# Kernel tuning notes

Measured on AMD Instinct MI355X. Metric: run time of the kernel, lower is better.

## Reference

```python
import jax, jax.numpy as jnp
import numpy as np

B = 64
N_TEXT, N_VIS, N_AC = 256, 32, 32
N = N_TEXT + N_VIS + N_AC  # 320 total graph nodes
HID, HEADS, LAYERS = 512, 8, 2
HEAD_DIM = HID // HEADS
SW_K, SW_P, SF_M, ALPHA, CROSS_P = 6, 0.15, 3, 0.5, 0.3


def build_hybrid_adj():
    """Watts-Strogatz + Barabasi-Albert hybrid adjacency with cross-modal edges (numpy, setup only)."""
    rng = np.random.default_rng(0)
    # small-world ring lattice
    sw = np.zeros((N, N), np.float32)
    idx = np.arange(N)
    for j in range(1, SW_K // 2 + 1):
        sw[idx, (idx + j) % N] = 1.0
        sw[idx, (idx - j) % N] = 1.0
    # rewiring
    for i in range(N):
        for j in range(i + 1, N):
            if sw[i, j] == 1 and rng.random() < SW_P:
                sw[i, j] = sw[j, i] = 0.0
                cand = np.where(sw[i] == 0)[0]
                cand = cand[cand != i]
                if len(cand) > 0:
                    nj = rng.choice(cand)
                    sw[i, nj] = sw[nj, i] = 1.0
    # scale-free (Barabasi-Albert)
    sf = np.zeros((N, N), np.float32)
    for i in range(SF_M + 1):
        for j in range(i + 1, SF_M + 1):
            sf[i, j] = sf[j, i] = 1.0
    deg = sf.sum(1)
    for v in range(SF_M + 1, N):
        prob = deg[:v] / deg[:v].sum()
        targets = rng.choice(v, size=min(SF_M, v), replace=False, p=prob)
        sf[v, targets] = 1.0
        sf[targets, v] = 1.0
        deg = sf.sum(1)
    adj = ((ALPHA * sw + (1.0 - ALPHA) * sf) > 0.3).astype(np.float32)
    # cross-modal edges: text<->visual, text<->acoustic (Bernoulli), visual<->acoustic temporal diagonal
    ts, te = 0, N_TEXT
    vs, ve = te, te + N_VIS
    as_, ae = ve, ve + N_AC
    cm_v = (rng.random((N_TEXT, N_VIS)) < CROSS_P).astype(np.float32)
    adj[ts:te, vs:ve] = np.maximum(adj[ts:te, vs:ve], cm_v)
    adj[vs:ve, ts:te] = adj[ts:te, vs:ve].T
    cm_a = (rng.random((N_TEXT, N_AC)) < CROSS_P).astype(np.float32)
    adj[ts:te, as_:ae] = np.maximum(adj[ts:te, as_:ae], cm_a)
    adj[as_:ae, ts:te] = adj[ts:te, as_:ae].T
    k = min(N_VIS, N_AC)
    adj[vs + np.arange(k), as_ + np.arange(k)] = 1.0
    adj[as_ + np.arange(k), vs + np.arange(k)] = 1.0
    return adj.astype(np.int32)


def setup_inputs() -> dict:
    key = jax.random.key(0)
    ks = jax.random.split(key, 12)
    s = 0.02
    return {
        "text": jax.random.normal(ks[0], (B, N_TEXT, 768), jnp.float32),
        "visual": jax.random.normal(ks[1], (B, N_VIS, 47), jnp.float32),
        "acoustic": jax.random.normal(ks[2], (B, N_AC, 74), jnp.float32),
        "adj": jnp.asarray(build_hybrid_adj()),
        "Wt": jax.random.normal(ks[3], (768, HID), jnp.float32) * s,
        "Wv": jax.random.normal(ks[4], (47, HID), jnp.float32) * s,
        "Wa": jax.random.normal(ks[5], (74, HID), jnp.float32) * s,
        "Wg": jax.random.normal(ks[6], (LAYERS, HEADS, HID, HEAD_DIM), jnp.float32) * s,
        "a_src": jax.random.normal(ks[7], (LAYERS, HEADS, HEAD_DIM), jnp.float32) * s,
        "a_dst": jax.random.normal(ks[8], (LAYERS, HEADS, HEAD_DIM), jnp.float32) * s,
        "edge_logits": jax.random.normal(ks[9], (N, N), jnp.float32) * s,
    }


def _fusion(text, visual, acoustic, adj, Wt, Wv, Wa, Wg, a_src, a_dst, edge_logits):
    # project each modality into shared hidden space and stack as graph nodes
    x = jnp.concatenate([
        jnp.einsum("btd,dh->bth", text, Wt),
        jnp.einsum("bvd,dh->bvh", visual, Wv),
        jnp.einsum("bad,dh->bah", acoustic, Wa),
    ], axis=1)  # [B, N, HID]
    mask = (adj != 0)[None, None, :, :]  # [1,1,N,N]
    for l in range(LAYERS):
        h = jnp.einsum("bnd,hdf->bhnf", x, Wg[l])          # [B,H,N,Fh]
        # a([h_i || h_j]) factorizes: e_ij = a_src.h_i + a_dst.h_j
        fi = jnp.einsum("bhnf,hf->bhn", h, a_src[l])
        fj = jnp.einsum("bhnf,hf->bhn", h, a_dst[l])
        e = jax.nn.leaky_relu(fi[:, :, :, None] + fj[:, :, None, :], 0.2)
        e = e + edge_logits[None, None, :, :]               # learnable topology bias
        e = jnp.where(mask, e, -jnp.inf)                    # adjacency-masked scores
        att = jnp.nan_to_num(jax.nn.softmax(e, axis=-1))    # fully-masked rows -> 0
        out = jnp.einsum("bhij,bhjf->bhif", att, h)         # message passing
        x = out.transpose(0, 2, 1, 3).reshape(x.shape[0], N, HID)  # concat heads
        if l < LAYERS - 1:
            x = jax.nn.elu(x)
    return x  # [B, N, HID] fused node embeddings


def reference(text, visual, acoustic, adj, Wt, Wv, Wa, Wg, a_src, a_dst, edge_logits):
    return _fusion(text, visual, acoustic, adj, Wt, Wv, Wa, Wg, a_src, a_dst, edge_logits)
```

## Files before the change

### kernel.cpp

```cpp
#include <hip/hip_runtime.h>
#include <hip/hip_bf16.h>
#include <math.h>

#define BB 64
#define NN 320
#define NT 256
#define NV 32
#define NA 32
#define HIDD 512
#define NHEAD 8
#define FD 64

typedef __attribute__((ext_vector_type(8))) short bf16x8;
typedef __attribute__((ext_vector_type(4))) float floatx4;

__device__ float me_g[NN * NN];
__device__ float fif_g[512 * NN];
__device__ float fjf_g[512 * NN];
__device__ unsigned short tihi_g[16384 * 768];
__device__ unsigned short tilo_g[16384 * 768];
__device__ unsigned short vihi_g[2048 * 64];
__device__ unsigned short vilo_g[2048 * 64];
__device__ unsigned short achi_g[2048 * 128];
__device__ unsigned short aclo_g[2048 * 128];
__device__ unsigned short xhi_g[20480 * 512];
__device__ unsigned short xlo_g[20480 * 512];
__device__ unsigned short bwhi_g[512 * 768];
__device__ unsigned short bwlo_g[512 * 768];

__device__ __forceinline__ void split1(float v, unsigned short& h, unsigned short& l) {
    unsigned u = __float_as_uint(v);
    unsigned hu = u & 0xFFFF0000u;
    float lf = v - __uint_as_float(hu);
    h = (unsigned short)(hu >> 16);
    l = (unsigned short)(__float_as_uint(lf) >> 16);
}
__device__ __forceinline__ unsigned pack2(unsigned short a, unsigned short b) {
    return (unsigned)a | ((unsigned)b << 16);
}

typedef const __attribute__((address_space(1))) unsigned int* gas1_t;
typedef __attribute__((address_space(3))) unsigned int* las3_t;
__device__ __forceinline__ void gload_lds16(const void* g, void* s) {
    __builtin_amdgcn_global_load_lds((gas1_t)(unsigned long long)g,
                                     (las3_t)(unsigned)(unsigned long long)s,
                                     16, 0, 0);
}

__global__ __launch_bounds__(256) void build_me(
    const int* __restrict__ adj, const float* __restrict__ elog)
{
    const int i4 = (blockIdx.x * 256 + threadIdx.x) * 4;
    const int4   a = *(const int4*)&adj[i4];
    const float4 e = *(const float4*)&elog[i4];
    float4 m;
    m.x = a.x ? __expf(e.x) : 0.f;
    m.y = a.y ? __expf(e.y) : 0.f;
    m.z = a.z ? __expf(e.z) : 0.f;
    m.w = a.w ? __expf(e.w) : 0.f;
    *(float4*)&me_g[i4] = m;
}

__global__ __launch_bounds__(256) void presplit_A(
    const float* __restrict__ src, int M, int K, int nk, int sel)
{
    unsigned short* dh = (sel == 0) ? tihi_g : (sel == 1) ? vihi_g : achi_g;
    unsigned short* dl = (sel == 0) ? tilo_g : (sel == 1) ? vilo_g : aclo_g;
    const unsigned t = blockIdx.x * 256 + threadIdx.x;
    const unsigned lane = t & 63, rec = t >> 6;
    const unsigned kt = rec % (unsigned)nk, g = rec / (unsigned)nk;
    const int row = g * 16 + (lane & 15);
    if (row >= M) return;
    const int k0 = kt * 32 + ((lane >> 4) << 3);
    float v[8];
    if (((K & 3) == 0) && (k0 + 8 <= K)) {
        *(float4*)&v[0] = *(const float4*)&src[(size_t)row * K + k0];
        *(float4*)&v[4] = *(const float4*)&src[(size_t)row * K + k0 + 4];
    } else {
#pragma unroll
        for (int e = 0; e < 8; e++) v[e] = (k0 + e < K) ? src[(size_t)row * K + k0 + e] : 0.f;
    }
    unsigned short h[8], l[8];
#pragma unroll
    for (int e = 0; e < 8; e++) split1(v[e], h[e], l[e]);
    const size_t o = (size_t)t * 8;
    *(uint4*)&dh[o] = make_uint4(pack2(h[0],h[1]), pack2(h[2],h[3]),
                                 pack2(h[4],h[5]), pack2(h[6],h[7]));
    *(uint4*)&dl[o] = make_uint4(pack2(l[0],l[1]), pack2(l[2],l[3]),
                                 pack2(l[4],l[5]), pack2(l[6],l[7]));
}

__global__ __launch_bounds__(64) void presplit_B(
    const float* __restrict__ W, int K, int Kp, int wg_mode)
{
    const int lane = threadIdx.x;
    const int nt = blockIdx.x, kt = blockIdx.y;
    const int col = nt * 16 + (lane & 15);
    const int k0 = kt * 32 + (lane >> 4) * 8;
    unsigned short h[8], l[8];
#pragma unroll
    for (int e = 0; e < 8; e++) {
        const int k = k0 + e;
        float v = 0.f;
        if (k < K) v = wg_mode ? W[(size_t)(col >> 6) * (512 * 64) + (size_t)k * 64 + (col & 63)]
                               : W[(size_t)k * 512 + col];
        split1(v, h[e], l[e]);
    }
    const size_t o = (((size_t)nt * (Kp >> 5) + kt) * 64 + lane) * 8;
    *(uint4*)&bwhi_g[o] = make_uint4(pack2(h[0], h[1]), pack2(h[2], h[3]),
                                     pack2(h[4], h[5]), pack2(h[6], h[7]));
    *(uint4*)&bwlo_g[o] = make_uint4(pack2(l[0], l[1]), pack2(l[2], l[3]),
                                     pack2(l[4], l[5]), pack2(l[6], l[7]));
}

#define GMFMA(AH, AL, BH, BL)                                                  \
  _Pragma("unroll") for (int s = 0; s < 4; s++)                                \
  _Pragma("unroll") for (int t = 0; t < 4; t++) {                              \
      acc[s][t] = __builtin_amdgcn_mfma_f32_16x16x32_bf16(AH[s], BH[t], acc[s][t], 0, 0, 0); \
      acc[s][t] = __builtin_amdgcn_mfma_f32_16x16x32_bf16(AH[s], BL[t], acc[s][t], 0, 0, 0); \
      acc[s][t] = __builtin_amdgcn_mfma_f32_16x16x32_bf16(AL[s], BH[t], acc[s][t], 0, 0, 0); }

__global__ __launch_bounds__(256, 2) void gemm_lds(
    unsigned short* __restrict__ Hthi, unsigned short* __restrict__ Htlo,
    const float* __restrict__ asrc, const float* __restrict__ adst,
    int nk, int a_sel, int b_mode, int rpb, int noff)
{
    __shared__ __align__(16) unsigned short stage[2][32 * 512];

    const unsigned short* Ahi = (a_sel == 0) ? tihi_g : (a_sel == 1) ? vihi_g
                              : (a_sel == 2) ? achi_g : xhi_g;
    const unsigned short* Alo = (a_sel == 0) ? tilo_g : (a_sel == 1) ? vilo_g
                              : (a_sel == 2) ? aclo_g : xlo_g;

    const int tid = threadIdx.x, lane = tid & 63, w = tid >> 6;
    const int rw = w >> 1, cw = w & 1;
    const int m0 = blockIdx.x * 128, n0 = blockIdx.y * 128;
    const int g0 = m0 >> 4, tg0 = n0 >> 4;

    const unsigned short* plane = (w == 0) ? Ahi : (w == 1) ? Alo
                                : (w == 2) ? bwhi_g : bwlo_g;
    const unsigned rec0 = (w < 2) ? (unsigned)g0 : (unsigned)tg0;
    const unsigned short* wsrc = plane + (size_t)rec0 * nk * 512 + lane * 8;
    const int woff = (w * 8) * 512;

    floatx4 acc[4][4];
#pragma unroll
    for (int s = 0; s < 4; s++)
#pragma unroll
        for (int t = 0; t < 4; t++) acc[s][t] = (floatx4)0.f;

#pragma unroll
    for (int u = 0; u < 8; u++)
        gload_lds16(wsrc + ((size_t)u * nk) * 512, &stage[0][woff + u * 512]);
    __syncthreads();

    int cur = 0;
    for (int kt = 0; kt < nk; ++kt) {
        if (kt + 1 < nk) {
            unsigned short* nb = &stage[cur ^ 1][woff];
#pragma unroll
            for (int u = 0; u < 8; u++)
                gload_lds16(wsrc + ((size_t)u * nk + kt + 1) * 512, nb + u * 512);
        }
        const unsigned short* sb = &stage[cur][0];
        bf16x8 a_h[4], a_l[4], b_h[4], b_l[4];
#pragma unroll
        for (int s = 0; s < 4; s++) {
            a_h[s] = *(const bf16x8*)&sb[(rw * 4 + s) * 512 + lane * 8];
            a_l[s] = *(const bf16x8*)&sb[(8 + rw * 4 + s) * 512 + lane * 8];
        }
#pragma unroll
        for (int t = 0; t < 4; t++) {
            b_h[t] = *(const bf16x8*)&sb[(16 + cw * 4 + t) * 512 + lane * 8];
            b_l[t] = *(const bf16x8*)&sb[(24 + cw * 4 + t) * 512 + lane * 8];
        }
        GMFMA(a_h, a_l, b_h, b_l);
        __syncthreads();
        cur ^= 1;
    }

    const int fq = lane & 15, rl = lane >> 4;

    if (b_mode == 0) {
        float (*sl)[68] = (float (*)[68])(&stage[0][w * 2176]);
        const int ktg0 = (n0 + cw * 64) >> 5;
#pragma unroll
        for (int s = 0; s < 4; s++) {
#pragma unroll
            for (int t = 0; t < 4; t++)
#pragma unroll
                for (int r = 0; r < 4; r++)
                    sl[rl * 4 + r][t * 16 + fq] = acc[s][t][r];
            const int grow16 = m0 + rw * 64 + s * 16;
            const int b = grow16 / rpb;
            const int rr = grow16 - b * rpb;
            const unsigned g = (unsigned)b * 20 + (unsigned)((noff + rr) >> 4);
#pragma unroll
            for (int kth = 0; kth < 2; kth++) {
                float f[8];
                *(float4*)&f[0] = *(const float4*)&sl[fq][kth * 32 + rl * 8];
                *(float4*)&f[4] = *(const float4*)&sl[fq][kth * 32 + rl * 8 + 4];
                unsigned short h[8], l[8];
#pragma unroll
                for (int e = 0; e < 8; e++) split1(f[e], h[e], l[e]);
                const size_t o = (((size_t)g * 16 + ktg0 + kth) * 64 + lane) * 8;
                *(uint4*)&xhi_g[o] = make_uint4(pack2(h[0],h[1]), pack2(h[2],h[3]),
                                                pack2(h[4],h[5]), pack2(h[6],h[7]));
                *(uint4*)&xlo_g[o] = make_uint4(pack2(l[0],l[1]), pack2(l[2],l[3]),
                                                pack2(l[4],l[5]), pack2(l[6],l[7]));
            }
        }
    } else {
        const int hd = (n0 + cw * 64) >> 6;
#pragma unroll
        for (int s = 0; s < 4; s++) {
            const int m_s = m0 + rw * 64 + s * 16 + rl * 4;
            const unsigned b = (unsigned)m_s / 320u;
            const int jb = m_s - b * 320;
            const int ks = jb >> 5;
            const int jg2 = (jb >> 3) & 3;
            const int eb = jb & 7;
            const size_t slabo = (size_t)b * 8 + hd;
#pragma unroll
            for (int t = 0; t < 4; t++) {
                unsigned short h0,h1,h2,h3,l0,l1,l2,l3;
                split1(acc[s][t][0],h0,l0); split1(acc[s][t][1],h1,l1);
                split1(acc[s][t][2],h2,l2); split1(acc[s][t][3],h3,l3);
                const size_t base = (((slabo * 10 + ks) * 4 + t) * 512
                                     + (size_t)(fq | (jg2 << 4)) * 8) + eb;
                *(uint2*)&Hthi[base] = make_uint2(pack2(h0,h1), pack2(h2,h3));
                *(uint2*)&Htlo[base] = make_uint2(pack2(l0,l1), pack2(l2,l3));
            }
        }
        float as4[4], ad4[4];
#pragma unroll
        for (int t = 0; t < 4; t++) {
            as4[t] = asrc[hd * 64 + t * 16 + fq];
            ad4[t] = adst[hd * 64 + t * 16 + fq];
        }
#pragma unroll
        for (int s = 0; s < 4; s++) {
            const int m_s = m0 + rw * 64 + s * 16 + rl * 4;
            const unsigned b = (unsigned)m_s / 320u;
            const int jb = m_s - b * 320;
            float4 fi4, fj4;
#pragma unroll
            for (int r = 0; r < 4; r++) {
                float fi = (acc[s][0][r]*as4[0] + acc[s][1][r]*as4[1])
                         + (acc[s][2][r]*as4[2] + acc[s][3][r]*as4[3]);
                float fj = (acc[s][0][r]*ad4[0] + acc[s][1][r]*ad4[1])
                         + (acc[s][2][r]*ad4[2] + acc[s][3][r]*ad4[3]);
#pragma unroll
                for (int d = 1; d < 16; d <<= 1) {
                    fi += __shfl_xor(fi, d);
                    fj += __shfl_xor(fj, d);
                }
                ((float*)&fi4)[r] = fi; ((float*)&fj4)[r] = fj;
            }
            if (fq == 0) {
                const size_t o = ((size_t)b * 8 + hd) * NN + jb;
                *(float4*)&fif_g[o] = fi4;
                *(float4*)&fjf_g[o] = fj4;
            }
        }
    }
}

template<int IP0, int NIP>
__device__ __forceinline__ void attn_body(
    const unsigned short* __restrict__ Hthi, const unsigned short* __restrict__ Htlo,
    float* __restrict__ xout, int final_out, float* fjs, float* ls,
    float (*slabA)[16][68])
{
    const int bh = blockIdx.x;
    const int hd = bh & 7, b = bh >> 3;
    const int tid = threadIdx.x, lane = tid & 63, w = tid >> 6;
    const int fq = lane & 15, jg = lane >> 4;

    for (int r = tid; r < NN; r += 256) fjs[r] = fjf_g[bh * NN + r];

    float fir[NIP];
#pragma unroll
    for (int ip = 0; ip < NIP; ip++)
        fir[ip] = fif_g[bh * NN + (IP0 + ip) * 64 + (w << 4) + fq];
    __syncthreads();

    floatx4 acc[NIP][4];
#pragma unroll
    for (int ip = 0; ip < NIP; ip++)
#pragma unroll
        for (int nt = 0; nt < 4; nt++) acc[ip][nt] = (floatx4)0.f;
    float lacc[NIP];
#pragma unroll
    for (int ip = 0; ip < NIP; ip++) lacc[ip] = 0.f;

    for (int ks = 0; ks < 10; ks++) {
        bf16x8 bhf[4], blf[4];
#pragma unroll
        for (int nt = 0; nt < 4; nt++) {
            const unsigned off = (((unsigned)bh * 10 + ks) * 4 + nt) * 512 + (unsigned)lane * 8;
            bhf[nt] = *(const bf16x8*)&Hthi[off];
            blf[nt] = *(const bf16x8*)&Htlo[off];
        }

        const int j8 = ks * 32 + jg * 8;
        const float4 fj0 = *(const float4*)&fjs[j8];
        const float4 fj1 = *(const float4*)&fjs[j8 + 4];

        bf16x8 ahh[NIP], all[NIP];
#pragma unroll
        for (int ip = 0; ip < NIP; ip++) {
            const int i = (IP0 + ip) * 64 + (w << 4) + fq;
            const float fiv = fir[ip];
            const unsigned g = (unsigned)i * NN + j8;
            const float4 m0 = *(const float4*)&me_g[g];
            const float4 m1 = *(const float4*)&me_g[g + 4];
            float p[8];
            {
                float s;
                s = fiv + fj0.x; s = fmaxf(s, 0.2f*s); p[0] = __expf(s) * m0.x;
                s = fiv + fj0.y; s = fmaxf(s, 0.2f*s); p[1] = __expf(s) * m0.y;
                s = fiv + fj0.z; s = fmaxf(s, 0.2f*s); p[2] = __expf(s) * m0.z;
                s = fiv + fj0.w; s = fmaxf(s, 0.2f*s); p[3] = __expf(s) * m0.w;
                s = fiv + fj1.x; s = fmaxf(s, 0.2f*s); p[4] = __expf(s) * m1.x;
                s = fiv + fj1.y; s = fmaxf(s, 0.2f*s); p[5] = __expf(s) * m1.y;
                s = fiv + fj1.z; s = fmaxf(s, 0.2f*s); p[6] = __expf(s) * m1.z;
                s = fiv + fj1.w; s = fmaxf(s, 0.2f*s); p[7] = __expf(s) * m1.w;
            }
            lacc[ip] += ((p[0]+p[1]) + (p[2]+p[3])) + ((p[4]+p[5]) + (p[6]+p[7]));

            unsigned short ph[8], pl[8];
#pragma unroll
            for (int e = 0; e < 8; e++) split1(p[e], ph[e], pl[e]);
            union { uint4 u; bf16x8 v; } ua, ul;
            ua.u = make_uint4(pack2(ph[0],ph[1]), pack2(ph[2],ph[3]),
                              pack2(ph[4],ph[5]), pack2(ph[6],ph[7]));
            ul.u = make_uint4(pack2(pl[0],pl[1]), pack2(pl[2],pl[3]),
                              pack2(pl[4],pl[5]), pack2(pl[6],pl[7]));
            ahh[ip] = ua.v; all[ip] = ul.v;
        }

        __builtin_amdgcn_s_setprio(1);
#pragma unroll
        for (int nt = 0; nt < 4; nt++)
#pragma unroll
            for (int ip = 0; ip < NIP; ip++) {
                acc[ip][nt] = __builtin_amdgcn_mfma_f32_16x16x32_bf16(ahh[ip], bhf[nt], acc[ip][nt], 0, 0, 0);
                acc[ip][nt] = __builtin_amdgcn_mfma_f32_16x16x32_bf16(ahh[ip], blf[nt], acc[ip][nt], 0, 0, 0);
                acc[ip][nt] = __builtin_amdgcn_mfma_f32_16x16x32_bf16(all[ip], bhf[nt], acc[ip][nt], 0, 0, 0);
            }
        __builtin_amdgcn_s_setprio(0);
    }

#pragma unroll
    for (int ip = 0; ip < NIP; ip++) {
        float l = lacc[ip];
        l += __shfl_xor(l, 16);
        l += __shfl_xor(l, 32);
        if (jg == 0) ls[(IP0 + ip) * 64 + (w << 4) + fq] = l;
    }
    __syncthreads();

    if (final_out) {
#pragma unroll
        for (int ip = 0; ip < NIP; ip++) {
            const int ib = ((IP0 + ip) * 4 + w) * 16 + jg * 4;
#pragma unroll
            for (int r = 0; r < 4; r++) {
                const float lv = ls[ib + r];
                const float inv = (lv > 0.f) ? 1.f / lv : 0.f;
                const size_t ro = ((size_t)(b * NN + ib + r)) * HIDD + hd * 64;
#pragma unroll
                for (int nt = 0; nt < 4; nt++)
                    xout[ro + nt * 16 + fq] = acc[ip][nt][r] * inv;
            }
        }
    } else {
        float (*sl)[68] = slabA[w];
        const int ktg0 = hd * 2;
#pragma unroll
        for (int ip = 0; ip < NIP; ip++) {
            const int ib = ((IP0 + ip) * 4 + w) * 16 + jg * 4;
#pragma unroll
            for (int r = 0; r < 4; r++) {
                const float lv = ls[ib + r];
                const float inv = (lv > 0.f) ? 1.f / lv : 0.f;
#pragma unroll
                for (int nt = 0; nt < 4; nt++) {
                    float vv = acc[ip][nt][r] * inv;
                    vv = (vv > 0.f) ? vv : __expf(vv) - 1.f;
                    sl[jg * 4 + r][nt * 16 + fq] = vv;
                }
            }
            const unsigned g = (unsigned)b * 20 + (IP0 + ip) * 4 + w;
#pragma unroll
            for (int kth = 0; kth < 2; kth++) {
                float f[8];
                *(float4*)&f[0] = *(const float4*)&sl[fq][kth * 32 + jg * 8];
                *(float4*)&f[4] = *(const float4*)&sl[fq][kth * 32 + jg * 8 + 4];
                unsigned short h[8], l[8];
#pragma unroll
                for (int e = 0; e < 8; e++) split1(f[e], h[e], l[e]);
                const size_t o = (((size_t)g * 16 + ktg0 + kth) * 64 + lane) * 8;
                *(uint4*)&xhi_g[o] = make_uint4(pack2(h[0],h[1]), pack2(h[2],h[3]),
                                                pack2(h[4],h[5]), pack2(h[6],h[7]));
                *(uint4*)&xlo_g[o] = make_uint4(pack2(l[0],l[1]), pack2(l[2],l[3]),
                                                pack2(l[4],l[5]), pack2(l[6],l[7]));
            }
        }
    }
}

__global__ __launch_bounds__(256, 4) void attn_mfma(
    const unsigned short* __restrict__ Hthi, const unsigned short* __restrict__ Htlo,
    float* __restrict__ xout, int final_out)
{
    __shared__ float fjs[NN];
    __shared__ float ls[NN];
    __shared__ float slabA[4][16][68];
    if (blockIdx.y == 0) attn_body<0, 3>(Hthi, Htlo, xout, final_out, fjs, ls, slabA);
    else                 attn_body<3, 2>(Hthi, Htlo, xout, final_out, fjs, ls, slabA);
}

extern "C" void kernel_launch(void* const* d_in, const int* in_sizes, int n_in,
                              void* d_out, int out_size, void* d_ws, size_t ws_size,
                              hipStream_t stream)
{
    (void)in_sizes; (void)n_in; (void)out_size; (void)ws_size;
    const float* text     = (const float*)d_in[0];
    const float* visual   = (const float*)d_in[1];
    const float* acoustic = (const float*)d_in[2];
    const int*   adj      = (const int*)d_in[3];
    const float* Wt       = (const float*)d_in[4];
    const float* Wv       = (const float*)d_in[5];
    const float* Wa       = (const float*)d_in[6];
    const float* Wg       = (const float*)d_in[7];
    const float* a_src    = (const float*)d_in[8];
    const float* a_dst    = (const float*)d_in[9];
    const float* elog     = (const float*)d_in[10];

    float* xbuf = (float*)d_out;
    unsigned short* Hthi = (unsigned short*)d_ws;
    unsigned short* Htlo = Hthi + (size_t)512 * 10 * 4 * 512;

    build_me<<<NN * NN / 1024, 256, 0, stream>>>(adj, elog);

    presplit_A<<<(16384 / 16) * 24 * 64 / 256, 256, 0, stream>>>(text,     16384, 768, 24, 0);
    presplit_A<<<(2048  / 16) * 2  * 64 / 256, 256, 0, stream>>>(visual,   2048,  47,  2,  1);
    presplit_A<<<(2048  / 16) * 4  * 64 / 256, 256, 0, stream>>>(acoustic, 2048,  74,  4,  2);

    presplit_B<<<dim3(32, 768 / 32), 64, 0, stream>>>(Wt, 768, 768, 0);
    gemm_lds<<<dim3((BB*NT)/128, 4), 256, 0, stream>>>(nullptr, nullptr, nullptr, nullptr,
                                                       24, 0, 0, NT, 0);
    presplit_B<<<dim3(32, 64 / 32), 64, 0, stream>>>(Wv, 47, 64, 0);
    gemm_lds<<<dim3((BB*NV)/128, 4), 256, 0, stream>>>(nullptr, nullptr, nullptr, nullptr,
                                                       2, 1, 0, NV, NT);
    presplit_B<<<dim3(32, 128 / 32), 64, 0, stream>>>(Wa, 74, 128, 0);
    gemm_lds<<<dim3((BB*NA)/128, 4), 256, 0, stream>>>(nullptr, nullptr, nullptr, nullptr,
                                                       4, 2, 0, NA, NT + NV);

    for (int l = 0; l < 2; l++) {
        const float* Wg_l = Wg + (size_t)l * NHEAD * HIDD * FD;
        presplit_B<<<dim3(32, 512 / 32), 64, 0, stream>>>(Wg_l, 512, 512, 1);
        gemm_lds<<<dim3((BB*NN)/128, 4), 256, 0, stream>>>(Hthi, Htlo,
            a_src + l * NHEAD * FD, a_dst + l * NHEAD * FD, 16, 3, 1, NN, 0);
        attn_mfma<<<dim3(BB * NHEAD, 2), 256, 0, stream>>>(
            Hthi, Htlo, xbuf, (l == 0) ? 0 : 1);
    }
}
```

Baseline: 406.1 us.

## Split attention kernel into one 64-row tile per block across five y-blocks

The attention kernel now assigns each block a single 64-row slice of query nodes (grid y=5) instead of splitting rows unevenly 3/2 across two blocks. Row sums are reduced and broadcast with warp shuffles instead of a shared-memory array and a barrier. The launch bound is raised to 6 blocks per CU for more occupancy. Each H tile is now loaded by five blocks instead of two, which adds redundant global/L2 traffic, and register-level reuse of B fragments across row tiles is lost.

```diff
diff --git a/kernel.cpp b/kernel.cpp
--- a/kernel.cpp
+++ b/kernel.cpp
@@ -266,160 +266,117 @@
     }
 }
 
-template<int IP0, int NIP>
-__device__ __forceinline__ void attn_body(
+__global__ __launch_bounds__(256, 6) void attn_mfma(
     const unsigned short* __restrict__ Hthi, const unsigned short* __restrict__ Htlo,
-    float* __restrict__ xout, int final_out, float* fjs, float* ls,
-    float (*slabA)[16][68])
-{
+    float* __restrict__ xout, int final_out)
+{
+    __shared__ float fjs[NN];
+    __shared__ float slabA[4][16][68];
+
     const int bh = blockIdx.x;
+    const int ip = blockIdx.y;
     const int hd = bh & 7, b = bh >> 3;
     const int tid = threadIdx.x, lane = tid & 63, w = tid >> 6;
     const int fq = lane & 15, jg = lane >> 4;
 
     for (int r = tid; r < NN; r += 256) fjs[r] = fjf_g[bh * NN + r];
-
-    float fir[NIP];
-#pragma unroll
-    for (int ip = 0; ip < NIP; ip++)
-        fir[ip] = fif_g[bh * NN + (IP0 + ip) * 64 + (w << 4) + fq];
+    const float fiv = fif_g[bh * NN + ip * 64 + (w << 4) + fq];
     __syncthreads();
 
-    floatx4 acc[NIP][4];
-#pragma unroll
-    for (int ip = 0; ip < NIP; ip++)
-#pragma unroll
-        for (int nt = 0; nt < 4; nt++) acc[ip][nt] = (floatx4)0.f;
-    float lacc[NIP];
-#pragma unroll
-    for (int ip = 0; ip < NIP; ip++) lacc[ip] = 0.f;
+    floatx4 acc[4];
+#pragma unroll
+    for (int nt = 0; nt < 4; nt++) acc[nt] = (floatx4)0.f;
+    float lacc = 0.f;
 
     for (int ks = 0; ks < 10; ks++) {
-        bf16x8 bhf[4], blf[4];
-#pragma unroll
-        for (int nt = 0; nt < 4; nt++) {
-            const unsigned off = (((unsigned)bh * 10 + ks) * 4 + nt) * 512 + (unsigned)lane * 8;
-            bhf[nt] = *(const bf16x8*)&Hthi[off];
-            blf[nt] = *(const bf16x8*)&Htlo[off];
-        }
-
         const int j8 = ks * 32 + jg * 8;
         const float4 fj0 = *(const float4*)&fjs[j8];
         const float4 fj1 = *(const float4*)&fjs[j8 + 4];
 
-        bf16x8 ahh[NIP], all[NIP];
-#pragma unroll
-        for (int ip = 0; ip < NIP; ip++) {
-            const int i = (IP0 + ip) * 64 + (w << 4) + fq;
-            const float fiv = fir[ip];
-            const unsigned g = (unsigned)i * NN + j8;
-            const float4 m0 = *(const float4*)&me_g[g];
-            const float4 m1 = *(const float4*)&me_g[g + 4];
-            float p[8];
-            {
-                float s;
-                s = fiv + fj0.x; s = fmaxf(s, 0.2f*s); p[0] = __expf(s) * m0.x;
-                s = fiv + fj0.y; s = fmaxf(s, 0.2f*s); p[1] = __expf(s) * m0.y;
-                s = fiv + fj0.z; s = fmaxf(s, 0.2f*s); p[2] = __expf(s) * m0.z;
-                s = fiv + fj0.w; s = fmaxf(s, 0.2f*s); p[3] = __expf(s) * m0.w;
-                s = fiv + fj1.x; s = fmaxf(s, 0.2f*s); p[4] = __expf(s) * m1.x;
-                s = fiv + fj1.y; s = fmaxf(s, 0.2f*s); p[5] = __expf(s) * m1.y;
-                s = fiv + fj1.z; s = fmaxf(s, 0.2f*s); p[6] = __expf(s) * m1.z;
-                s = fiv + fj1.w; s = fmaxf(s, 0.2f*s); p[7] = __expf(s) * m1.w;
-            }
-            lacc[ip] += ((p[0]+p[1]) + (p[2]+p[3])) + ((p[4]+p[5]) + (p[6]+p[7]));
-
-            unsigned short ph[8], pl[8];
-#pragma unroll
-            for (int e = 0; e < 8; e++) split1(p[e], ph[e], pl[e]);
-            union { uint4 u; bf16x8 v; } ua, ul;
-            ua.u = make_uint4(pack2(ph[0],ph[1]), pack2(ph[2],ph[3]),
-                              pack2(ph[4],ph[5]), pack2(ph[6],ph[7]));
-            ul.u = make_uint4(pack2(pl[0],pl[1]), pack2(pl[2],pl[3]),
-                              pack2(pl[4],pl[5]), pack2(pl[6],pl[7]));
-            ahh[ip] = ua.v; all[ip] = ul.v;
-        }
+        const unsigned g = (unsigned)(ip * 64 + (w << 4) + fq) * NN + j8;
+        const float4 m0 = *(const float4*)&me_g[g];
+        const float4 m1 = *(const float4*)&me_g[g + 4];
+        float p[8];
+        {
+            float s;
+            s = fiv + fj0.x; s = fmaxf(s, 0.2f*s); p[0] = __expf(s) * m0.x;
+            s = fiv + fj0.y; s = fmaxf(s, 0.2f*s); p[1] = __expf(s) * m0.y;
+            s = fiv + fj0.z; s = fmaxf(s, 0.2f*s); p[2] = __expf(s) * m0.z;
+            s = fiv + fj0.w; s = fmaxf(s, 0.2f*s); p[3] = __expf(s) * m0.w;
+            s = fiv + fj1.x; s = fmaxf(s, 0.2f*s); p[4] = __expf(s) * m1.x;
+            s = fiv + fj1.y; s = fmaxf(s, 0.2f*s); p[5] = __expf(s) * m1.y;
+            s = fiv + fj1.z; s = fmaxf(s, 0.2f*s); p[6] = __expf(s) * m1.z;
+            s = fiv + fj1.w; s = fmaxf(s, 0.2f*s); p[7] = __expf(s) * m1.w;
+        }
+        lacc += ((p[0]+p[1]) + (p[2]+p[3])) + ((p[4]+p[5]) + (p[6]+p[7]));
+
+        unsigned short ph[8], pl[8];
+#pragma unroll
+        for (int e = 0; e < 8; e++) split1(p[e], ph[e], pl[e]);
+        union { uint4 u; bf16x8 v; } ua, ul;
+        ua.u = make_uint4(pack2(ph[0],ph[1]), pack2(ph[2],ph[3]),
+                          pack2(ph[4],ph[5]), pack2(ph[6],ph[7]));
+        ul.u = make_uint4(pack2(pl[0],pl[1]), pack2(pl[2],pl[3]),
+                          pack2(pl[4],pl[5]), pack2(pl[6],pl[7]));
+        const bf16x8 ahh = ua.v, all = ul.v;
 
         __builtin_amdgcn_s_setprio(1);
 #pragma unroll
-        for (int nt = 0; nt < 4; nt++)
-#pragma unroll
-            for (int ip = 0; ip < NIP; ip++) {
-                acc[ip][nt] = __builtin_amdgcn_mfma_f32_16x16x32_bf16(ahh[ip], bhf[nt], acc[ip][nt], 0, 0, 0);
-                acc[ip][nt] = __builtin_amdgcn_mfma_f32_16x16x32_bf16(ahh[ip], blf[nt], acc[ip][nt], 0, 0, 0);
-                acc[ip][nt] = __builtin_amdgcn_mfma_f32_16x16x32_bf16(all[ip], bhf[nt], acc[ip][nt], 0, 0, 0);
-            }
+        for (int nt = 0; nt < 4; nt++) {
+            const unsigned off = (((unsigned)bh * 10 + ks) * 4 + nt) * 512 + (unsigned)lane * 8;
+            const bf16x8 bhf = *(const bf16x8*)&Hthi[off];
+            const bf16x8 blf = *(const bf16x8*)&Htlo[off];
+            acc[nt] = __builtin_amdgcn_mfma_f32_16x16x32_bf16(ahh, bhf, acc[nt], 0, 0, 0);
+            acc[nt] = __builtin_amdgcn_mfma_f32_16x16x32_bf16(ahh, blf, acc[nt], 0, 0, 0);
+            acc[nt] = __builtin_amdgcn_mfma_f32_16x16x32_bf16(all, bhf, acc[nt], 0, 0, 0);
+        }
         __builtin_amdgcn_s_setprio(0);
     }
 
-#pragma unroll
-    for (int ip = 0; ip < NIP; ip++) {
-        float l = lacc[ip];
-        l += __shfl_xor(l, 16);
-        l += __shfl_xor(l, 32);
-        if (jg == 0) ls[(IP0 + ip) * 64 + (w << 4) + fq] = l;
-    }
-    __syncthreads();
+    lacc += __shfl_xor(lacc, 16);
+    lacc += __shfl_xor(lacc, 32);
 
     if (final_out) {
 #pragma unroll
-        for (int ip = 0; ip < NIP; ip++) {
-            const int ib = ((IP0 + ip) * 4 + w) * 16 + jg * 4;
-#pragma unroll
-            for (int r = 0; r < 4; r++) {
-                const float lv = ls[ib + r];
-                const float inv = (lv > 0.f) ? 1.f / lv : 0.f;
-                const size_t ro = ((size_t)(b * NN + ib + r)) * HIDD + hd * 64;
-#pragma unroll
-                for (int nt = 0; nt < 4; nt++)
-                    xout[ro + nt * 16 + fq] = acc[ip][nt][r] * inv;
-            }
+        for (int r = 0; r < 4; r++) {
+            const float lv = __shfl(lacc, jg * 4 + r);
+            const float inv = (lv > 0.f) ? 1.f / lv : 0.f;
+            const int ib = (ip * 4 + w) * 16 + jg * 4 + r;
+            const size_t ro = ((size_t)(b * NN + ib)) * HIDD + hd * 64;
+#pragma unroll
+            for (int nt = 0; nt < 4; nt++)
+                xout[ro + nt * 16 + fq] = acc[nt][r] * inv;
         }
     } else {
         float (*sl)[68] = slabA[w];
         const int ktg0 = hd * 2;
 #pragma unroll
-        for (int ip = 0; ip < NIP; ip++) {
-            const int ib = ((IP0 + ip) * 4 + w) * 16 + jg * 4;
-#pragma unroll
-            for (int r = 0; r < 4; r++) {
-                const float lv = ls[ib + r];
-                const float inv = (lv > 0.f) ? 1.f / lv : 0.f;
-#pragma unroll
-                for (int nt = 0; nt < 4; nt++) {
-                    float vv = acc[ip][nt][r] * inv;
-                    vv = (vv > 0.f) ? vv : __expf(vv) - 1.f;
-                    sl[jg * 4 + r][nt * 16 + fq] = vv;
-                }
+        for (int r = 0; r < 4; r++) {
+            const float lv = __shfl(lacc, jg * 4 + r);
+            const float inv = (lv > 0.f) ? 1.f / lv : 0.f;
+#pragma unroll
+            for (int nt = 0; nt < 4; nt++) {
+                float vv = acc[nt][r] * inv;
+                vv = (vv > 0.f) ? vv : __expf(vv) - 1.f;
+                sl[jg * 4 + r][nt * 16 + fq] = vv;
             }
-            const unsigned g = (unsigned)b * 20 + (IP0 + ip) * 4 + w;
-#pragma unroll
-            for (int kth = 0; kth < 2; kth++) {
-                float f[8];
-                *(float4*)&f[0] = *(const float4*)&sl[fq][kth * 32 + jg * 8];
-                *(float4*)&f[4] = *(const float4*)&sl[fq][kth * 32 + jg * 8 + 4];
-                unsigned short h[8], l[8];
-#pragma unroll
-                for (int e = 0; e < 8; e++) split1(f[e], h[e], l[e]);
-                const size_t o = (((size_t)g * 16 + ktg0 + kth) * 64 + lane) * 8;
-                *(uint4*)&xhi_g[o] = make_uint4(pack2(h[0],h[1]), pack2(h[2],h[3]),
-                                                pack2(h[4],h[5]), pack2(h[6],h[7]));
-                *(uint4*)&xlo_g[o] = make_uint4(pack2(l[0],l[1]), pack2(l[2],l[3]),
-                                                pack2(l[4],l[5]), pack2(l[6],l[7]));
-            }
-        }
-    }
-}
-
-__global__ __launch_bounds__(256, 4) void attn_mfma(
-    const unsigned short* __restrict__ Hthi, const unsigned short* __restrict__ Htlo,
-    float* __restrict__ xout, int final_out)
-{
-    __shared__ float fjs[NN];
-    __shared__ float ls[NN];
-    __shared__ float slabA[4][16][68];
-    if (blockIdx.y == 0) attn_body<0, 3>(Hthi, Htlo, xout, final_out, fjs, ls, slabA);
-    else                 attn_body<3, 2>(Hthi, Htlo, xout, final_out, fjs, ls, slabA);
+        }
+        const unsigned g = (unsigned)b * 20 + ip * 4 + w;
+#pragma unroll
+        for (int kth = 0; kth < 2; kth++) {
+            float f[8];
+            *(float4*)&f[0] = *(const float4*)&sl[fq][kth * 32 + jg * 8];
+            *(float4*)&f[4] = *(const float4*)&sl[fq][kth * 32 + jg * 8 + 4];
+            unsigned short h[8], l[8];
+#pragma unroll
+            for (int e = 0; e < 8; e++) split1(f[e], h[e], l[e]);
+            const size_t o = (((size_t)g * 16 + ktg0 + kth) * 64 + lane) * 8;
+            *(uint4*)&xhi_g[o] = make_uint4(pack2(h[0],h[1]), pack2(h[2],h[3]),
+                                            pack2(h[4],h[5]), pack2(h[6],h[7]));
+            *(uint4*)&xlo_g[o] = make_uint4(pack2(l[0],l[1]), pack2(l[2],l[3]),
+                                            pack2(l[4],l[5]), pack2(l[6],l[7]));
+        }
+    }
 }
 
 extern "C" void kernel_launch(void* const* d_in, const int* in_sizes, int n_in,
@@ -464,7 +421,7 @@
         presplit_B<<<dim3(32, 512 / 32), 64, 0, stream>>>(Wg_l, 512, 512, 1);
         gemm_lds<<<dim3((BB*NN)/128, 4), 256, 0, stream>>>(Hthi, Htlo,
             a_src + l * NHEAD * FD, a_dst + l * NHEAD * FD, 16, 3, 1, NN, 0);
-        attn_mfma<<<dim3(BB * NHEAD, 2), 256, 0, stream>>>(
+        attn_mfma<<<dim3(BB * NHEAD, 5), 256, 0, stream>>>(
             Hthi, Htlo, xbuf, (l == 0) ? 0 : 1);
     }
 }
```

New measurement: 386.0 us. 5.0% less time.

## Merge weight presplits and prep kernels, fuse visual/acoustic GEMMs, drop LDS row sums

Applied to the files above, without the earlier changes.

All weight presplits plus the adjacency/exp mask build are merged into one prep_w launch that writes into a larger, offset-indexed split-weight buffer. Visual and acoustic presplit and GEMM are each merged into single launches, so the launch count drops from about 14 to 7. The attention kernel now broadcasts softmax row sums with shuffles instead of an LDS array and a __syncthreads, and its occupancy hint is lowered from 4 to 3. The aim is to cut launch gaps and serialization between small kernels, at the cost of a larger weight buffer and more branching inside the kernels.

```diff
diff --git a/kernel.cpp b/kernel.cpp
--- a/kernel.cpp
+++ b/kernel.cpp
@@ -25,8 +25,8 @@
 __device__ unsigned short aclo_g[2048 * 128];
 __device__ unsigned short xhi_g[20480 * 512];
 __device__ unsigned short xlo_g[20480 * 512];
-__device__ unsigned short bwhi_g[512 * 768];
-__device__ unsigned short bwlo_g[512 * 768];
+__device__ unsigned short bwhi_g[1015808];
+__device__ unsigned short bwlo_g[1015808];
 
 __device__ __forceinline__ void split1(float v, unsigned short& h, unsigned short& l) {
     unsigned u = __float_as_uint(v);
@@ -47,26 +47,58 @@
                                      16, 0, 0);
 }
 
-__global__ __launch_bounds__(256) void build_me(
+__global__ __launch_bounds__(64) void prep_w(
+    const float* __restrict__ Wt, const float* __restrict__ Wv,
+    const float* __restrict__ Wa, const float* __restrict__ Wg,
     const int* __restrict__ adj, const float* __restrict__ elog)
 {
-    const int i4 = (blockIdx.x * 256 + threadIdx.x) * 4;
-    const int4   a = *(const int4*)&adj[i4];
-    const float4 e = *(const float4*)&elog[i4];
-    float4 m;
-    m.x = a.x ? __expf(e.x) : 0.f;
-    m.y = a.y ? __expf(e.y) : 0.f;
-    m.z = a.z ? __expf(e.z) : 0.f;
-    m.w = a.w ? __expf(e.w) : 0.f;
-    *(float4*)&me_g[i4] = m;
-}
-
-__global__ __launch_bounds__(256) void presplit_A(
-    const float* __restrict__ src, int M, int K, int nk, int sel)
-{
-    unsigned short* dh = (sel == 0) ? tihi_g : (sel == 1) ? vihi_g : achi_g;
-    unsigned short* dl = (sel == 0) ? tilo_g : (sel == 1) ? vilo_g : aclo_g;
-    const unsigned t = blockIdx.x * 256 + threadIdx.x;
+    const int x = blockIdx.x, y = blockIdx.y;
+    const int lane = threadIdx.x;
+
+    if (y >= 62) {
+        const int i4 = (((y - 62) * 32 + x) * 64 + lane) * 4;
+        if (i4 < NN * NN) {
+            const int4   a = *(const int4*)&adj[i4];
+            const float4 e = *(const float4*)&elog[i4];
+            float4 m;
+            m.x = a.x ? __expf(e.x) : 0.f;
+            m.y = a.y ? __expf(e.y) : 0.f;
+            m.z = a.z ? __expf(e.z) : 0.f;
+            m.w = a.w ? __expf(e.w) : 0.f;
+            *(float4*)&me_g[i4] = m;
+        }
+        return;
+    }
+
+    int kt, nk, K, wgm; const float* W; size_t base;
+    if (y < 24)      { kt = y;      nk = 24; K = 768; wgm = 0; W = Wt; base = 0; }
+    else if (y < 26) { kt = y - 24; nk = 2;  K = 47;  wgm = 0; W = Wv; base = 393216; }
+    else if (y < 30) { kt = y - 26; nk = 4;  K = 74;  wgm = 0; W = Wa; base = 425984; }
+    else if (y < 46) { kt = y - 30; nk = 16; K = 512; wgm = 1; W = Wg; base = 491520; }
+    else             { kt = y - 46; nk = 16; K = 512; wgm = 1; W = Wg + 262144; base = 753664; }
+
+    const int col = x * 16 + (lane & 15);
+    const int k0 = kt * 32 + (lane >> 4) * 8;
+    unsigned short h[8], l[8];
+#pragma unroll
+    for (int e = 0; e < 8; e++) {
+        const int k = k0 + e;
+        float v = 0.f;
+        if (k < K) v = wgm ? W[(size_t)(col >> 6) * (512 * 64) + (size_t)k * 64 + (col & 63)]
+                           : W[(size_t)k * 512 + col];
+        split1(v, h[e], l[e]);
+    }
+    const size_t o = base + (((size_t)x * nk + kt) * 64 + lane) * 8;
+    *(uint4*)&bwhi_g[o] = make_uint4(pack2(h[0], h[1]), pack2(h[2], h[3]),
+                                     pack2(h[4], h[5]), pack2(h[6], h[7]));
+    *(uint4*)&bwlo_g[o] = make_uint4(pack2(l[0], l[1]), pack2(l[2], l[3]),
+                                     pack2(l[4], l[5]), pack2(l[6], l[7]));
+}
+
+__device__ __forceinline__ void presplitA_body(
+    const float* __restrict__ src, int M, int K, int nk,
+    unsigned short* __restrict__ dh, unsigned short* __restrict__ dl, unsigned t)
+{
     const unsigned lane = t & 63, rec = t >> 6;
     const unsigned kt = rec % (unsigned)nk, g = rec / (unsigned)nk;
     const int row = g * 16 + (lane & 15);
@@ -90,27 +122,18 @@
                                  pack2(l[4],l[5]), pack2(l[6],l[7]));
 }
 
-__global__ __launch_bounds__(64) void presplit_B(
-    const float* __restrict__ W, int K, int Kp, int wg_mode)
-{
-    const int lane = threadIdx.x;
-    const int nt = blockIdx.x, kt = blockIdx.y;
-    const int col = nt * 16 + (lane & 15);
-    const int k0 = kt * 32 + (lane >> 4) * 8;
-    unsigned short h[8], l[8];
-#pragma unroll
-    for (int e = 0; e < 8; e++) {
-        const int k = k0 + e;
-        float v = 0.f;
-        if (k < K) v = wg_mode ? W[(size_t)(col >> 6) * (512 * 64) + (size_t)k * 64 + (col & 63)]
-                               : W[(size_t)k * 512 + col];
-        split1(v, h[e], l[e]);
-    }
-    const size_t o = (((size_t)nt * (Kp >> 5) + kt) * 64 + lane) * 8;
-    *(uint4*)&bwhi_g[o] = make_uint4(pack2(h[0], h[1]), pack2(h[2], h[3]),
-                                     pack2(h[4], h[5]), pack2(h[6], h[7]));
-    *(uint4*)&bwlo_g[o] = make_uint4(pack2(l[0], l[1]), pack2(l[2], l[3]),
-                                     pack2(l[4], l[5]), pack2(l[6], l[7]));
+__global__ __launch_bounds__(256) void presplit_text(const float* __restrict__ src)
+{
+    presplitA_body(src, 16384, 768, 24, tihi_g, tilo_g, blockIdx.x * 256 + threadIdx.x);
+}
+
+__global__ __launch_bounds__(256) void prep_va(
+    const float* __restrict__ visual, const float* __restrict__ acoustic)
+{
+    if (blockIdx.x < 64)
+        presplitA_body(visual, 2048, 47, 2, vihi_g, vilo_g, blockIdx.x * 256 + threadIdx.x);
+    else
+        presplitA_body(acoustic, 2048, 74, 4, achi_g, aclo_g, (blockIdx.x - 64) * 256 + threadIdx.x);
 }
 
 #define GMFMA(AH, AL, BH, BL)                                                  \
@@ -123,9 +146,15 @@
 __global__ __launch_bounds__(256, 2) void gemm_lds(
     unsigned short* __restrict__ Hthi, unsigned short* __restrict__ Htlo,
     const float* __restrict__ asrc, const float* __restrict__ adst,
-    int nk, int a_sel, int b_mode, int rpb, int noff)
+    int nk, int a_sel, int bwoff, int b_mode, int rpb, int noff, int merged_va)
 {
     __shared__ __align__(16) unsigned short stage[2][32 * 512];
+
+    int mb = blockIdx.x;
+    if (merged_va) {
+        if (mb < 16) { a_sel = 1; nk = 2; bwoff = 393216; noff = NT; }
+        else { mb -= 16; a_sel = 2; nk = 4; bwoff = 425984; noff = NT + NV; }
+    }
 
     const unsigned short* Ahi = (a_sel == 0) ? tihi_g : (a_sel == 1) ? vihi_g
                               : (a_sel == 2) ? achi_g : xhi_g;
@@ -134,11 +163,11 @@
 
     const int tid = threadIdx.x, lane = tid & 63, w = tid >> 6;
     const int rw = w >> 1, cw = w & 1;
-    const int m0 = blockIdx.x * 128, n0 = blockIdx.y * 128;
+    const int m0 = mb * 128, n0 = blockIdx.y * 128;
     const int g0 = m0 >> 4, tg0 = n0 >> 4;
 
     const unsigned short* plane = (w == 0) ? Ahi : (w == 1) ? Alo
-                                : (w == 2) ? bwhi_g : bwlo_g;
+                                : (w == 2) ? (bwhi_g + bwoff) : (bwlo_g + bwoff);
     const unsigned rec0 = (w < 2) ? (unsigned)g0 : (unsigned)tg0;
     const unsigned short* wsrc = plane + (size_t)rec0 * nk * 512 + lane * 8;
     const int woff = (w * 8) * 512;
@@ -269,7 +298,7 @@
 template<int IP0, int NIP>
 __device__ __forceinline__ void attn_body(
     const unsigned short* __restrict__ Hthi, const unsigned short* __restrict__ Htlo,
-    float* __restrict__ xout, int final_out, float* fjs, float* ls,
+    float* __restrict__ xout, int final_out, float* fjs,
     float (*slabA)[16][68])
 {
     const int bh = blockIdx.x;
@@ -310,9 +339,8 @@
         bf16x8 ahh[NIP], all[NIP];
 #pragma unroll
         for (int ip = 0; ip < NIP; ip++) {
-            const int i = (IP0 + ip) * 64 + (w << 4) + fq;
             const float fiv = fir[ip];
-            const unsigned g = (unsigned)i * NN + j8;
+            const unsigned g = (unsigned)((IP0 + ip) * 64 + (w << 4) + fq) * NN + j8;
             const float4 m0 = *(const float4*)&me_g[g];
             const float4 m1 = *(const float4*)&me_g[g + 4];
             float p[8];
@@ -354,36 +382,31 @@
 
 #pragma unroll
     for (int ip = 0; ip < NIP; ip++) {
-        float l = lacc[ip];
-        l += __shfl_xor(l, 16);
-        l += __shfl_xor(l, 32);
-        if (jg == 0) ls[(IP0 + ip) * 64 + (w << 4) + fq] = l;
-    }
-    __syncthreads();
+        lacc[ip] += __shfl_xor(lacc[ip], 16);
+        lacc[ip] += __shfl_xor(lacc[ip], 32);
+    }
 
     if (final_out) {
 #pragma unroll
-        for (int ip = 0; ip < NIP; ip++) {
-            const int ib = ((IP0 + ip) * 4 + w) * 16 + jg * 4;
+        for (int ip = 0; ip < NIP; ip++)
 #pragma unroll
             for (int r = 0; r < 4; r++) {
-                const float lv = ls[ib + r];
+                const float lv = __shfl(lacc[ip], jg * 4 + r);
                 const float inv = (lv > 0.f) ? 1.f / lv : 0.f;
-                const size_t ro = ((size_t)(b * NN + ib + r)) * HIDD + hd * 64;
+                const int ib = ((IP0 + ip) * 4 + w) * 16 + jg * 4 + r;
+                const size_t ro = ((size_t)(b * NN + ib)) * HIDD + hd * 64;
 #pragma unroll
                 for (int nt = 0; nt < 4; nt++)
                     xout[ro + nt * 16 + fq] = acc[ip][nt][r] * inv;
             }
-        }
     } else {
         float (*sl)[68] = slabA[w];
         const int ktg0 = hd * 2;
 #pragma unroll
         for (int ip = 0; ip < NIP; ip++) {
-            const int ib = ((IP0 + ip) * 4 + w) * 16 + jg * 4;
 #pragma unroll
             for (int r = 0; r < 4; r++) {
-                const float lv = ls[ib + r];
+                const float lv = __shfl(lacc[ip], jg * 4 + r);
                 const float inv = (lv > 0.f) ? 1.f / lv : 0.f;
 #pragma unroll
                 for (int nt = 0; nt < 4; nt++) {
@@ -411,15 +434,14 @@
     }
 }
 
-__global__ __launch_bounds__(256, 4) void attn_mfma(
+__global__ __launch_bounds__(256, 3) void attn_mfma(
     const unsigned short* __restrict__ Hthi, const unsigned short* __restrict__ Htlo,
     float* __restrict__ xout, int final_out)
 {
     __shared__ float fjs[NN];
-    __shared__ float ls[NN];
     __shared__ float slabA[4][16][68];
-    if (blockIdx.y == 0) attn_body<0, 3>(Hthi, Htlo, xout, final_out, fjs, ls, slabA);
-    else                 attn_body<3, 2>(Hthi, Htlo, xout, final_out, fjs, ls, slabA);
+    if (blockIdx.y == 0) attn_body<0, 3>(Hthi, Htlo, xout, final_out, fjs, slabA);
+    else                 attn_body<3, 2>(Hthi, Htlo, xout, final_out, fjs, slabA);
 }
 
 extern "C" void kernel_launch(void* const* d_in, const int* in_sizes, int n_in,
@@ -443,27 +465,19 @@
     unsigned short* Hthi = (unsigned short*)d_ws;
     unsigned short* Htlo = Hthi + (size_t)512 * 10 * 4 * 512;
 
-    build_me<<<NN * NN / 1024, 256, 0, stream>>>(adj, elog);
-
-    presplit_A<<<(16384 / 16) * 24 * 64 / 256, 256, 0, stream>>>(text,     16384, 768, 24, 0);
-    presplit_A<<<(2048  / 16) * 2  * 64 / 256, 256, 0, stream>>>(visual,   2048,  47,  2,  1);
-    presplit_A<<<(2048  / 16) * 4  * 64 / 256, 256, 0, stream>>>(acoustic, 2048,  74,  4,  2);
-
-    presplit_B<<<dim3(32, 768 / 32), 64, 0, stream>>>(Wt, 768, 768, 0);
+    prep_w<<<dim3(32, 75), 64, 0, stream>>>(Wt, Wv, Wa, Wg, adj, elog);
+    presplit_text<<<6144, 256, 0, stream>>>(text);
+    prep_va<<<192, 256, 0, stream>>>(visual, acoustic);
+
     gemm_lds<<<dim3((BB*NT)/128, 4), 256, 0, stream>>>(nullptr, nullptr, nullptr, nullptr,
-                                                       24, 0, 0, NT, 0);
-    presplit_B<<<dim3(32, 64 / 32), 64, 0, stream>>>(Wv, 47, 64, 0);
-    gemm_lds<<<dim3((BB*NV)/128, 4), 256, 0, stream>>>(nullptr, nullptr, nullptr, nullptr,
-                                                       2, 1, 0, NV, NT);
-    presplit_B<<<dim3(32, 128 / 32), 64, 0, stream>>>(Wa, 74, 128, 0);
-    gemm_lds<<<dim3((BB*NA)/128, 4), 256, 0, stream>>>(nullptr, nullptr, nullptr, nullptr,
-                                                       4, 2, 0, NA, NT + NV);
+                                                       24, 0, 0, 0, NT, 0, 0);
+    gemm_lds<<<dim3(32, 4), 256, 0, stream>>>(nullptr, nullptr, nullptr, nullptr,
+                                              0, 0, 0, 0, 32, 0, 1);
 
     for (int l = 0; l < 2; l++) {
-        const float* Wg_l = Wg + (size_t)l * NHEAD * HIDD * FD;
-        presplit_B<<<dim3(32, 512 / 32), 64, 0, stream>>>(Wg_l, 512, 512, 1);
         gemm_lds<<<dim3((BB*NN)/128, 4), 256, 0, stream>>>(Hthi, Htlo,
-            a_src + l * NHEAD * FD, a_dst + l * NHEAD * FD, 16, 3, 1, NN, 0);
+            a_src + l * NHEAD * FD, a_dst + l * NHEAD * FD,
+            16, 3, (l == 0) ? 491520 : 753664, 1, NN, 0, 0);
         attn_mfma<<<dim3(BB * NHEAD, 2), 256, 0, stream>>>(
             Hthi, Htlo, xbuf, (l == 0) ? 0 : 1);
     }
```

Result: faster. 345.4 us (-15.0%).
